# Kernel optimization log

Measured on AMD Instinct MI355X. Metric: run time of the kernel, lower is better.

Reference implementation:

```python
import jax, jax.numpy as jnp
import numpy as np
import math

NUM_BANDS = 16
BINS = 1024
CROPSIZE = 1024
BATCH = 4


def setup_inputs() -> dict:
    key = jax.random.key(0)
    ks = jax.random.split(key, 10)
    s = 1.0 / math.sqrt(BINS)
    return {
        "x": jax.random.normal(ks[0], (BATCH, CROPSIZE, BINS), jnp.float32),
        "Wq": jax.random.normal(ks[1], (BINS, BINS), jnp.float32) * s,
        "bq": jax.random.normal(ks[2], (BINS,), jnp.float32) * 0.02,
        "Wk": jax.random.normal(ks[3], (BINS, BINS), jnp.float32) * s,
        "bk": jax.random.normal(ks[4], (BINS,), jnp.float32) * 0.02,
        "Wv": jax.random.normal(ks[5], (BINS, BINS), jnp.float32) * s,
        "bv": jax.random.normal(ks[6], (BINS,), jnp.float32) * 0.02,
        "Wo": jax.random.normal(ks[7], (BINS, BINS), jnp.float32) * s,
        "bo": jax.random.normal(ks[8], (BINS,), jnp.float32) * 0.02,
        "er": jax.random.normal(ks[9], (BINS // NUM_BANDS, CROPSIZE), jnp.float32),
    }


def reference(x, Wq, bq, Wk, bk, Wv, bv, Wo, bo, er):
    b, w, c = x.shape
    h = NUM_BANDS
    d = c // h
    # Linear projections (torch Linear: x @ W.T + b)
    q = (jnp.einsum("bwc,oc->bwo", x, Wq) + bq).reshape(b, w, h, d).transpose(0, 2, 1, 3)  # [b,h,w,d]
    k = (jnp.einsum("bwc,oc->bwo", x, Wk) + bk).reshape(b, w, h, d).transpose(0, 2, 1, 3)  # [b,h,w,d]
    v = (jnp.einsum("bwc,oc->bwo", x, Wv) + bv).reshape(b, w, h, d).transpose(0, 2, 1, 3)  # [b,h,w,d]
    # relative-position bias via skew trick
    qe = jnp.einsum("bhwd,dc->bhwc", q, er)  # [b,h,w,cropsize]
    qe = jnp.pad(qe, ((0, 0), (0, 0), (0, 0), (1, 0)))  # pad last dim on left -> [b,h,w,crop+1]
    p = jnp.swapaxes(qe, 2, 3)[:, :, 1:, :]  # [b,h,crop,w] == [b,h,w,w] since crop==w
    qk = (jnp.einsum("bhwd,bhud->bhwu", q, k) + p) / math.sqrt(c)
    a = jax.nn.softmax(qk, axis=-1)
    av = jnp.einsum("bhwu,bhud->bhwd", a, v).transpose(0, 2, 1, 3).reshape(b, w, c)
    return jnp.einsum("bwc,oc->bwo", av, Wo) + bo
```

## Files before the change

kernel.cpp:

```cpp
#include <hip/hip_runtime.h>
#include <stdint.h>

typedef __attribute__((ext_vector_type(8))) short   short8;
typedef __attribute__((ext_vector_type(8))) __bf16  bf16x8;
typedef __attribute__((ext_vector_type(4))) float   floatx4;

__device__ __forceinline__ float bf2f(uint16_t h) {
    union { uint32_t u; float f; } v; v.u = ((uint32_t)h) << 16; return v.f;
}
__device__ __forceinline__ uint16_t f2bf(float f) {
    union { float f; uint32_t u; } v; v.f = f;
    uint32_t u = v.u;
    u += 0x7FFFu + ((u >> 16) & 1u);
    return (uint16_t)(u >> 16);
}
__device__ __forceinline__ floatx4 mfma16(short8 a, short8 b, floatx4 c) {
    return __builtin_amdgcn_mfma_f32_16x16x32_bf16(
        __builtin_bit_cast(bf16x8, a), __builtin_bit_cast(bf16x8, b), c, 0, 0, 0);
}
__device__ __forceinline__ void gll16(const short* g, short* l) {
    __builtin_amdgcn_global_load_lds(
        (const __attribute__((address_space(1))) uint32_t*)g,
        (__attribute__((address_space(3))) uint32_t*)l, 16, 0, 0);
}

__global__ void conv_all(
    const float* __restrict__ x,
    const float* __restrict__ Wq, const float* __restrict__ Wk,
    const float* __restrict__ Wv, const float* __restrict__ Wo,
    const float* __restrict__ bq, const float* __restrict__ bk,
    const float* __restrict__ bv, const float* __restrict__ bo,
    const float* __restrict__ er,
    short* __restrict__ xb, short* __restrict__ Wb,
    short* __restrict__ ball, short* __restrict__ ErT)
{
    int blk = blockIdx.x, tid = threadIdx.x;
    if (blk < 4096) {
        int i = blk * 256 + tid;
        float4 v = ((const float4*)x)[i];
        ((short4*)xb)[i] = make_short4((short)f2bf(v.x), (short)f2bf(v.y),
                                       (short)f2bf(v.z), (short)f2bf(v.w));
    } else if (blk < 8192) {
        int rel = blk - 4096;
        int wsel = rel >> 10;
        int i = (rel & 1023) * 256 + tid;
        const float* W = (wsel == 0) ? Wq : (wsel == 1) ? Wk : (wsel == 2) ? Wv : Wo;
        float4 v = ((const float4*)W)[i];
        ((short4*)(Wb + ((size_t)wsel << 20)))[i] =
            make_short4((short)f2bf(v.x), (short)f2bf(v.y),
                        (short)f2bf(v.z), (short)f2bf(v.w));
    } else if (blk < 8448) {
        int idx = (blk - 8192) * 256 + tid;
        int w = idx >> 6, d = idx & 63;
        ErT[idx] = (short)f2bf(er[d * 1024 + w]);
    } else {
        int idx = (blk - 8448) * 256 + tid;
        int sel = idx >> 10, j = idx & 1023;
        const float* s = (sel == 0) ? bq : (sel == 1) ? bk : (sel == 2) ? bv : bo;
        ball[idx] = (short)f2bf(s[j]);
    }
}

__device__ __forceinline__ void gemm_body(
    const short* __restrict__ A, const short* __restrict__ Wt,
    const short* __restrict__ bias, short* __restrict__ dst,
    float* __restrict__ dstf, int variant)
{
    __shared__ short As[128 * 64];
    __shared__ short Bs[128 * 64];
    const int tid  = threadIdx.x;
    const int wid  = tid >> 6;
    const int lane = tid & 63;
    const int m0 = blockIdx.x * 128;
    const int n0 = blockIdx.y * 128;
    const int wm = (wid >> 1) * 64;
    const int wn = (wid & 1) * 64;
    const int lrow = lane & 15;
    const int quad = lane >> 4;
    const int srow = lane >> 3;
    const int sscol = (((lane & 7) ^ (srow & 7)) << 3);
    const int rx = lrow & 7;

    floatx4 acc[4][4];
#pragma unroll
    for (int r = 0; r < 4; ++r)
#pragma unroll
        for (int c = 0; c < 4; ++c) acc[r][c] = (floatx4){0.f, 0.f, 0.f, 0.f};

    for (int k0 = 0; k0 < 1024; k0 += 64) {
#pragma unroll
        for (int i = 0; i < 4; ++i) {
            int q = wid * 4 + i;
            gll16(A + (size_t)(m0 + q * 8 + srow) * 1024 + k0 + sscol,
                  &As[q * 512 + lane * 8]);
        }
#pragma unroll
        for (int i = 0; i < 4; ++i) {
            int q = wid * 4 + i;
            gll16(Wt + (size_t)(n0 + q * 8 + srow) * 1024 + k0 + sscol,
                  &Bs[q * 512 + lane * 8]);
        }
        __syncthreads();
#pragma unroll
        for (int ks = 0; ks < 2; ++ks) {
            short8 af[4], bfr[4];
#pragma unroll
            for (int r = 0; r < 4; ++r)
                af[r] = *(const short8*)&As[(wm + r * 16 + lrow) * 64 +
                                            (((ks * 4 + quad) ^ rx) << 3)];
#pragma unroll
            for (int c = 0; c < 4; ++c)
                bfr[c] = *(const short8*)&Bs[(wn + c * 16 + lrow) * 64 +
                                             (((ks * 4 + quad) ^ rx) << 3)];
#pragma unroll
            for (int r = 0; r < 4; ++r)
#pragma unroll
                for (int c = 0; c < 4; ++c)
                    acc[r][c] = mfma16(af[r], bfr[c], acc[r][c]);
        }
        __syncthreads();
    }

#pragma unroll
    for (int c = 0; c < 4; ++c) {
        int col = n0 + wn + c * 16 + lrow;
        float bv = bf2f((uint16_t)bias[col]);
#pragma unroll
        for (int r = 0; r < 4; ++r) {
#pragma unroll
            for (int g = 0; g < 4; ++g) {
                int m = m0 + wm + r * 16 + quad * 4 + g;
                float fv = acc[r][c][g] + bv;
                if (variant == 3) {
                    dstf[(size_t)m * 1024 + col] = fv;
                } else if (variant == 2) {
                    int bh = (m >> 10) * 16 + (col >> 6);
                    dst[(size_t)bh * 65536 + (size_t)(col & 63) * 1024 + (m & 1023)] =
                        (short)f2bf(fv);
                } else {
                    int bh = (m >> 10) * 16 + (col >> 6);
                    dst[(size_t)bh * 65536 + (size_t)(m & 1023) * 64 + (col & 63)] =
                        (short)f2bf(fv);
                }
            }
        }
    }
}

__global__ __launch_bounds__(256) void out_gemm(
    const short* __restrict__ AV, const short* __restrict__ Wo,
    const short* __restrict__ bo, float* __restrict__ out)
{
    gemm_body(AV, Wo, bo, nullptr, out, 3);
}

#define VM0  asm volatile("s_waitcnt vmcnt(0)" ::: "memory")
#define BARR asm volatile("s_barrier" ::: "memory")

__device__ __forceinline__ void stage_unit(const short* src, short* region, int tid)
{
    const int row  = tid >> 3;
    const int scol = (((tid & 7) ^ (row & 7)) << 3);
    gll16(src + (size_t)row * 1024 + scol, region + tid * 8);
}

#define SAU(buf, u) (As + (buf) * 16384 + (u) * 4096)
#define SBU(buf, u) (Bs + (buf) * 12288 + (u) * 4096)
#define STG_A(buf, u, kt) stage_unit(Asrc + (size_t)(u) * 65536 + (size_t)(kt) * 64, SAU(buf, u), tid)
#define STG_B(buf, u, kt) stage_unit(Bsrc + (size_t)(u) * 65536 + (size_t)(kt) * 64, SBU(buf, u), tid)
#define STG7(buf, kt) do { \
    STG_A(buf, 0, kt); STG_A(buf, 1, kt); STG_A(buf, 2, kt); STG_A(buf, 3, kt); \
    STG_B(buf, 0, kt); STG_B(buf, 1, kt); STG_B(buf, 2, kt); } while (0)

#define RD_A(buf) do { \
    _Pragma("unroll") for (int fr_ = 0; fr_ < 8; ++fr_) { \
        const short* p_ = SAU(buf, wm * 2 + (fr_ >> 2)) + ((fr_ & 3) * 16 + lrow) * 64; \
        _Pragma("unroll") for (int ks_ = 0; ks_ < 2; ++ks_) \
            a[fr_][ks_] = *(const short8*)&p_[((ks_ * 4 + quad) ^ rx) << 3]; \
    } } while (0)

#define RD_B(buf, c) do { \
    const short* p_ = SBU(buf, c) + (wn * 16 + lrow) * 64; \
    _Pragma("unroll") for (int ks_ = 0; ks_ < 2; ++ks_) \
        bb[ks_] = *(const short8*)&p_[((ks_ * 4 + quad) ^ rx) << 3]; \
    } while (0)

#define MFMA_PH(c) do { \
    __builtin_amdgcn_s_setprio(1); \
    _Pragma("unroll") for (int ks_ = 0; ks_ < 2; ++ks_) \
        _Pragma("unroll") for (int fr_ = 0; fr_ < 8; ++fr_) \
            acc[fr_][c] = mfma16(a[fr_][ks_], bb[ks_], acc[fr_][c]); \
    __builtin_amdgcn_s_setprio(0); \
    } while (0)

__global__ __launch_bounds__(512, 2) void qkv_gemm2ph(
    const short* __restrict__ x, const short* __restrict__ Wb,
    const short* __restrict__ ball,
    short* __restrict__ Qb, short* __restrict__ Kb, short* __restrict__ Vb)
{
    extern __shared__ short lds[];
    short* As = lds;
    short* Bs = lds + 32768;
    const int tid  = threadIdx.x;
    const int wid  = tid >> 6;
    const int lane = tid & 63;
    const int wm   = wid >> 2;
    const int wn   = wid & 3;
    const int lrow = lane & 15;
    const int quad = lane >> 4;
    const int rx   = lrow & 7;
    const int bid  = blockIdx.x;
    const int swz  = (bid & 7) * 32 + (bid >> 3);
    const int mi   = swz & 15, ni = swz >> 4;
    const int m0   = mi * 256, n0 = ni * 192;
    const short* Asrc = x  + (size_t)m0 * 1024;
    const short* Bsrc = Wb + (size_t)n0 * 1024;

    floatx4 acc[8][3];
#pragma unroll
    for (int r = 0; r < 8; ++r)
#pragma unroll
        for (int c = 0; c < 3; ++c) acc[r][c] = (floatx4){0.f, 0.f, 0.f, 0.f};

    short8 a[8][2], bb[2];

    STG7(0, 0);
    VM0; BARR;

#pragma unroll 2
    for (int t = 0; t < 16; ++t) {
        const int cur = t & 1;
        if (t < 15) STG7(cur ^ 1, t + 1);
        RD_A(cur);
        RD_B(cur, 0); MFMA_PH(0);
        RD_B(cur, 1); MFMA_PH(1);
        RD_B(cur, 2); MFMA_PH(2);
        VM0; BARR;
    }

#pragma unroll
    for (int fc = 0; fc < 3; ++fc) {
        int col = n0 + fc * 64 + wn * 16 + lrow;
        int z   = col >> 10;
        int c1  = col & 1023;
        short* dst = (z == 0) ? Qb : (z == 1) ? Kb : Vb;
        float bv = bf2f((uint16_t)ball[col]);
#pragma unroll
        for (int fr = 0; fr < 8; ++fr) {
#pragma unroll
            for (int g = 0; g < 4; ++g) {
                int m = m0 + wm * 128 + fr * 16 + quad * 4 + g;
                float fv = acc[fr][fc][g] + bv;
                int bh = (m >> 10) * 16 + (c1 >> 6);
                if (z == 2)
                    dst[(size_t)bh * 65536 + (size_t)(c1 & 63) * 1024 + (m & 1023)] =
                        (short)f2bf(fv);
                else
                    dst[(size_t)bh * 65536 + (size_t)(m & 1023) * 64 + (c1 & 63)] =
                        (short)f2bf(fv);
            }
        }
    }
}

#define PSTR 72
__global__ __launch_bounds__(512, 4) void attn_kernel(
    const short* __restrict__ Q, const short* __restrict__ K,
    const short* __restrict__ Vt, const short* __restrict__ ErT,
    short* __restrict__ AV)
{
    __shared__ short smem[33792];
    short* Ks  = smem;
    short* Qks = smem + 8192;
    short* Vs  = smem + 16384;
    short* Ps  = smem + 24576;
    float* oaccS = (float*)smem;
    float* lrunS = ((float*)smem) + 128 * 65;

    const int tid  = threadIdx.x;
    const int wid  = tid >> 6;
    const int lane = tid & 63;
    const int rg   = wid >> 1;
    const int cg   = wid & 1;
    const int lrow = lane & 15;
    const int quad = lane >> 4;
    const int lk   = quad * 8;
    const int srow = lane >> 3;
    const int sscol = (((lane & 7) ^ (srow & 7)) << 3);
    const int rx = lrow & 7;
    const int h = blockIdx.x, b = blockIdx.y;
    const int bh = b * 16 + h;
    const int i0 = blockIdx.z * 128;
    const short* Qbh = Q  + (size_t)bh * 65536;
    const short* Kbh = K  + (size_t)bh * 65536;
    const short* Vbh = Vt + (size_t)bh * 65536;

    short8 qa[2][4];
#pragma unroll
    for (int m = 0; m < 2; ++m) {
        int row = i0 + rg * 32 + m * 16 + lrow;
#pragma unroll
        for (int kk = 0; kk < 2; ++kk) {
            qa[m][kk]     = *(const short8*)&Qbh[(size_t)row * 64 + kk * 32 + lk];
            qa[m][kk + 2] = *(const short8*)&ErT[(size_t)row * 64 + kk * 32 + lk];
        }
    }

    float lrun[2][4];
    floatx4 oacc[2][4];
#pragma unroll
    for (int m = 0; m < 2; ++m) {
#pragma unroll
        for (int g = 0; g < 4; ++g) lrun[m][g] = 0.f;
#pragma unroll
        for (int c = 0; c < 4; ++c) oacc[m][c] = (floatx4){0.f, 0.f, 0.f, 0.f};
    }

    gll16(Kbh + (size_t)(wid * 8 + srow) * 64 + sscol,    Ks  + wid * 512 + lane * 8);
    gll16(Qbh + (size_t)(wid * 8 + srow) * 64 + sscol,    Qks + wid * 512 + lane * 8);
    gll16(Vbh + (size_t)(wid * 8 + srow) * 1024 + sscol,  Vs  + wid * 512 + lane * 8);

    const float sc2 = 1.44269504088896f / 32.0f;

    for (int jt = 0; jt < 16; ++jt) {
        const int cur = jt & 1;
        __syncthreads();

        if (jt < 15) {
            int j1 = (jt + 1) * 64;
            gll16(Kbh + (size_t)(j1 + wid * 8 + srow) * 64 + sscol,    Ks  + (cur ^ 1) * 4096 + wid * 512 + lane * 8);
            gll16(Qbh + (size_t)(j1 + wid * 8 + srow) * 64 + sscol,    Qks + (cur ^ 1) * 4096 + wid * 512 + lane * 8);
            gll16(Vbh + (size_t)(wid * 8 + srow) * 1024 + j1 + sscol,  Vs  + (cur ^ 1) * 4096 + wid * 512 + lane * 8);
        }

        floatx4 s[2][2];
#pragma unroll
        for (int m = 0; m < 2; ++m)
#pragma unroll
            for (int c = 0; c < 2; ++c) s[m][c] = (floatx4){0.f, 0.f, 0.f, 0.f};
#pragma unroll
        for (int kk = 0; kk < 4; ++kk) {
            short8 kb[2];
            const short* src = ((kk < 2) ? Ks : Qks) + cur * 4096;
            const int kl = kk & 1;
#pragma unroll
            for (int c = 0; c < 2; ++c)
                kb[c] = *(const short8*)&src[(cg * 32 + c * 16 + lrow) * 64 +
                                             (((kl * 4 + quad) ^ rx) << 3)];
#pragma unroll
            for (int m = 0; m < 2; ++m)
#pragma unroll
                for (int c = 0; c < 2; ++c)
                    s[m][c] = mfma16(qa[m][kk], kb[c], s[m][c]);
        }

#pragma unroll
        for (int m = 0; m < 2; ++m)
#pragma unroll
            for (int c = 0; c < 2; ++c)
#pragma unroll
                for (int g = 0; g < 4; ++g)
                    s[m][c][g] = exp2f(s[m][c][g] * sc2);
#pragma unroll
        for (int m = 0; m < 2; ++m)
#pragma unroll
            for (int g = 0; g < 4; ++g)
                lrun[m][g] += s[m][0][g] + s[m][1][g];

#pragma unroll
        for (int m = 0; m < 2; ++m)
#pragma unroll
            for (int c = 0; c < 2; ++c)
#pragma unroll
                for (int g = 0; g < 4; ++g)
                    Ps[(rg * 32 + m * 16 + quad * 4 + g) * PSTR + cg * 32 + c * 16 + lrow] =
                        (short)f2bf(s[m][c][g]);
        __asm__ __volatile__("" ::: "memory");

        {
            short8 pa[2], vb[4];
#pragma unroll
            for (int m = 0; m < 2; ++m)
                pa[m] = *(const short8*)&Ps[(rg * 32 + m * 16 + lrow) * PSTR + cg * 32 + lk];
#pragma unroll
            for (int c = 0; c < 4; ++c)
                vb[c] = *(const short8*)&Vs[cur * 4096 + (c * 16 + lrow) * 64 +
                                            (((cg * 4 + quad) ^ rx) << 3)];
#pragma unroll
            for (int m = 0; m < 2; ++m)
#pragma unroll
                for (int c = 0; c < 4; ++c)
                    oacc[m][c] = mfma16(pa[m], vb[c], oacc[m][c]);
        }
    }

#pragma unroll
    for (int m = 0; m < 2; ++m)
#pragma unroll
        for (int g = 0; g < 4; ++g) {
            float r = lrun[m][g];
#pragma unroll
            for (int d = 1; d < 16; d <<= 1) r += __shfl_xor(r, d, 64);
            lrun[m][g] = r;
        }

    __syncthreads();
    if (cg == 0) {
#pragma unroll
        for (int m = 0; m < 2; ++m) {
#pragma unroll
            for (int c = 0; c < 4; ++c)
#pragma unroll
                for (int g = 0; g < 4; ++g)
                    oaccS[(rg * 32 + m * 16 + quad * 4 + g) * 65 + c * 16 + lrow] =
                        oacc[m][c][g];
            if (lrow == 0)
#pragma unroll
                for (int g = 0; g < 4; ++g)
                    lrunS[rg * 32 + m * 16 + quad * 4 + g] = lrun[m][g];
        }
    }
    __syncthreads();
    if (cg == 1) {
#pragma unroll
        for (int m = 0; m < 2; ++m)
#pragma unroll
            for (int g = 0; g < 4; ++g) {
                int row = rg * 32 + m * 16 + quad * 4 + g;
                float lt = lrun[m][g] + lrunS[row];
#pragma unroll
                for (int c = 0; c < 4; ++c) {
                    float tot = oacc[m][c][g] + oaccS[row * 65 + c * 16 + lrow];
                    AV[((size_t)b * 1024 + i0 + row) * 1024 + h * 64 + c * 16 + lrow] =
                        (short)f2bf(tot / lt);
                }
            }
    }
}

extern "C" void kernel_launch(void* const* d_in, const int* in_sizes, int n_in,
                              void* d_out, int out_size, void* d_ws, size_t ws_size,
                              hipStream_t stream) {
    const float* x  = (const float*)d_in[0];
    const float* Wq = (const float*)d_in[1];
    const float* bq = (const float*)d_in[2];
    const float* Wk = (const float*)d_in[3];
    const float* bk = (const float*)d_in[4];
    const float* Wv = (const float*)d_in[5];
    const float* bv = (const float*)d_in[6];
    const float* Wo = (const float*)d_in[7];
    const float* bo = (const float*)d_in[8];
    const float* er = (const float*)d_in[9];
    float* out = (float*)d_out;

    const size_t M1 = 1u << 20;
    short* ws   = (short*)d_ws;
    short* xb   = (short*)d_out;
    short* Qb   = ws;
    short* Kb   = ws + 4 * M1;
    short* Vb   = ws + 8 * M1;
    short* AVb  = ws + 12 * M1;
    short* Wb   = ws + 16 * M1;
    short* ball = ws + 20 * M1;
    short* ErT  = ws + 20 * M1 + 4096;

    static bool attr_done = false;
    if (!attr_done) {
        hipFuncSetAttribute((const void*)qkv_gemm2ph,
                            hipFuncAttributeMaxDynamicSharedMemorySize, 114688);
        attr_done = true;
    }

    hipLaunchKernelGGL(conv_all, dim3(8464), dim3(256), 0, stream,
                       x, Wq, Wk, Wv, Wo, bq, bk, bv, bo, er, xb, Wb, ball, ErT);
    hipLaunchKernelGGL(qkv_gemm2ph, dim3(256), dim3(512), 114688, stream,
                       xb, Wb, ball, Qb, Kb, Vb);
    hipLaunchKernelGGL(attn_kernel, dim3(16, 4, 8), dim3(512), 0, stream,
                       Qb, Kb, Vb, ErT, AVb);
    hipLaunchKernelGGL(out_gemm, dim3(32, 8), dim3(256), 0, stream,
                       AVb, Wb + 3 * M1, ball + 3072, out);
}
```

Before: 203.7 us.

## Replace output GEMM with double-buffered 512-thread kernel and XCD-aware tile mapping

Replaces the simple single-buffered 256-thread output projection GEMM with a 512-thread kernel. The new kernel prefetches the next K tile into a second LDS buffer while the current one is consumed by MFMAs, and raises wave priority around the MFMA bursts. It also remaps block IDs so blocks landing on the same XCD share A/B tiles in L2, and changes the QKV GEMM's tile mapping the same way. The aim is to hide global-load latency and improve L2 locality. The cost is more LDS per block and each wave holding a smaller 64x32 tile, which lowers MFMA reuse per LDS read.

```diff
diff --git a/kernel.cpp b/kernel.cpp
--- a/kernel.cpp
+++ b/kernel.cpp
@@ -61,99 +61,6 @@
     }
 }
 
-__device__ __forceinline__ void gemm_body(
-    const short* __restrict__ A, const short* __restrict__ Wt,
-    const short* __restrict__ bias, short* __restrict__ dst,
-    float* __restrict__ dstf, int variant)
-{
-    __shared__ short As[128 * 64];
-    __shared__ short Bs[128 * 64];
-    const int tid  = threadIdx.x;
-    const int wid  = tid >> 6;
-    const int lane = tid & 63;
-    const int m0 = blockIdx.x * 128;
-    const int n0 = blockIdx.y * 128;
-    const int wm = (wid >> 1) * 64;
-    const int wn = (wid & 1) * 64;
-    const int lrow = lane & 15;
-    const int quad = lane >> 4;
-    const int srow = lane >> 3;
-    const int sscol = (((lane & 7) ^ (srow & 7)) << 3);
-    const int rx = lrow & 7;
-
-    floatx4 acc[4][4];
-#pragma unroll
-    for (int r = 0; r < 4; ++r)
-#pragma unroll
-        for (int c = 0; c < 4; ++c) acc[r][c] = (floatx4){0.f, 0.f, 0.f, 0.f};
-
-    for (int k0 = 0; k0 < 1024; k0 += 64) {
-#pragma unroll
-        for (int i = 0; i < 4; ++i) {
-            int q = wid * 4 + i;
-            gll16(A + (size_t)(m0 + q * 8 + srow) * 1024 + k0 + sscol,
-                  &As[q * 512 + lane * 8]);
-        }
-#pragma unroll
-        for (int i = 0; i < 4; ++i) {
-            int q = wid * 4 + i;
-            gll16(Wt + (size_t)(n0 + q * 8 + srow) * 1024 + k0 + sscol,
-                  &Bs[q * 512 + lane * 8]);
-        }
-        __syncthreads();
-#pragma unroll
-        for (int ks = 0; ks < 2; ++ks) {
-            short8 af[4], bfr[4];
-#pragma unroll
-            for (int r = 0; r < 4; ++r)
-                af[r] = *(const short8*)&As[(wm + r * 16 + lrow) * 64 +
-                                            (((ks * 4 + quad) ^ rx) << 3)];
-#pragma unroll
-            for (int c = 0; c < 4; ++c)
-                bfr[c] = *(const short8*)&Bs[(wn + c * 16 + lrow) * 64 +
-                                             (((ks * 4 + quad) ^ rx) << 3)];
-#pragma unroll
-            for (int r = 0; r < 4; ++r)
-#pragma unroll
-                for (int c = 0; c < 4; ++c)
-                    acc[r][c] = mfma16(af[r], bfr[c], acc[r][c]);
-        }
-        __syncthreads();
-    }
-
-#pragma unroll
-    for (int c = 0; c < 4; ++c) {
-        int col = n0 + wn + c * 16 + lrow;
-        float bv = bf2f((uint16_t)bias[col]);
-#pragma unroll
-        for (int r = 0; r < 4; ++r) {
-#pragma unroll
-            for (int g = 0; g < 4; ++g) {
-                int m = m0 + wm + r * 16 + quad * 4 + g;
-                float fv = acc[r][c][g] + bv;
-                if (variant == 3) {
-                    dstf[(size_t)m * 1024 + col] = fv;
-                } else if (variant == 2) {
-                    int bh = (m >> 10) * 16 + (col >> 6);
-                    dst[(size_t)bh * 65536 + (size_t)(col & 63) * 1024 + (m & 1023)] =
-                        (short)f2bf(fv);
-                } else {
-                    int bh = (m >> 10) * 16 + (col >> 6);
-                    dst[(size_t)bh * 65536 + (size_t)(m & 1023) * 64 + (col & 63)] =
-                        (short)f2bf(fv);
-                }
-            }
-        }
-    }
-}
-
-__global__ __launch_bounds__(256) void out_gemm(
-    const short* __restrict__ AV, const short* __restrict__ Wo,
-    const short* __restrict__ bo, float* __restrict__ out)
-{
-    gemm_body(AV, Wo, bo, nullptr, out, 3);
-}
-
 #define VM0  asm volatile("s_waitcnt vmcnt(0)" ::: "memory")
 #define BARR asm volatile("s_barrier" ::: "memory")
 
@@ -210,8 +117,9 @@
     const int quad = lane >> 4;
     const int rx   = lrow & 7;
     const int bid  = blockIdx.x;
-    const int swz  = (bid & 7) * 32 + (bid >> 3);
-    const int mi   = swz & 15, ni = swz >> 4;
+    const int xcd  = bid & 7, gg = bid >> 3;
+    const int mi   = (xcd >> 1) * 4 + (gg & 3);
+    const int ni   = (xcd & 1) * 8 + (gg >> 2);
     const int m0   = mi * 256, n0 = ni * 192;
     const short* Asrc = x  + (size_t)m0 * 1024;
     const short* Bsrc = Wb + (size_t)n0 * 1024;
@@ -258,6 +166,93 @@
                 else
                     dst[(size_t)bh * 65536 + (size_t)(m & 1023) * 64 + (c1 & 63)] =
                         (short)f2bf(fv);
+            }
+        }
+    }
+}
+
+#define SAU2(buf, u) (As2 + (buf) * 8192 + (u) * 4096)
+#define SBU2(buf, u) (Bs2 + (buf) * 8192 + (u) * 4096)
+#define STG4(buf, kt) do { \
+    stage_unit(Asrc + 0 * 65536 + (size_t)(kt) * 64, SAU2(buf, 0), tid); \
+    stage_unit(Asrc + 1 * 65536 + (size_t)(kt) * 64, SAU2(buf, 1), tid); \
+    stage_unit(Bsrc + 0 * 65536 + (size_t)(kt) * 64, SBU2(buf, 0), tid); \
+    stage_unit(Bsrc + 1 * 65536 + (size_t)(kt) * 64, SBU2(buf, 1), tid); } while (0)
+
+#define RD_A2(buf) do { \
+    _Pragma("unroll") for (int fr_ = 0; fr_ < 4; ++fr_) { \
+        const short* p_ = SAU2(buf, wm) + (fr_ * 16 + lrow) * 64; \
+        _Pragma("unroll") for (int ks_ = 0; ks_ < 2; ++ks_) \
+            a[fr_][ks_] = *(const short8*)&p_[((ks_ * 4 + quad) ^ rx) << 3]; \
+    } } while (0)
+
+#define RD_B2(buf, c) do { \
+    const short* p_ = SBU2(buf, c) + (wn * 16 + lrow) * 64; \
+    _Pragma("unroll") for (int ks_ = 0; ks_ < 2; ++ks_) \
+        bb[ks_] = *(const short8*)&p_[((ks_ * 4 + quad) ^ rx) << 3]; \
+    } while (0)
+
+#define MFMA_PH2(c) do { \
+    __builtin_amdgcn_s_setprio(1); \
+    _Pragma("unroll") for (int ks_ = 0; ks_ < 2; ++ks_) \
+        _Pragma("unroll") for (int fr_ = 0; fr_ < 4; ++fr_) \
+            acc[fr_][c] = mfma16(a[fr_][ks_], bb[ks_], acc[fr_][c]); \
+    __builtin_amdgcn_s_setprio(0); \
+    } while (0)
+
+__global__ __launch_bounds__(512, 2) void out_gemm2ph(
+    const short* __restrict__ AV, const short* __restrict__ Wo,
+    const short* __restrict__ bo, float* __restrict__ out)
+{
+    __shared__ short As2[2 * 2 * 4096];
+    __shared__ short Bs2[2 * 2 * 4096];
+    const int tid  = threadIdx.x;
+    const int wid  = tid >> 6;
+    const int lane = tid & 63;
+    const int wm   = wid >> 2;
+    const int wn   = wid & 3;
+    const int lrow = lane & 15;
+    const int quad = lane >> 4;
+    const int rx   = lrow & 7;
+    const int bid  = blockIdx.x + blockIdx.y * 32;
+    const int xcd  = bid & 7, gg = bid >> 3;
+    const int mi   = (xcd & 3) * 8 + (gg & 7);
+    const int ni   = (xcd >> 2) * 4 + (gg >> 3);
+    const int m0   = mi * 128, n0 = ni * 128;
+    const short* Asrc = AV + (size_t)m0 * 1024;
+    const short* Bsrc = Wo + (size_t)n0 * 1024;
+
+    floatx4 acc[4][2];
+#pragma unroll
+    for (int r = 0; r < 4; ++r)
+#pragma unroll
+        for (int c = 0; c < 2; ++c) acc[r][c] = (floatx4){0.f, 0.f, 0.f, 0.f};
+
+    short8 a[4][2], bb[2];
+
+    STG4(0, 0);
+    VM0; BARR;
+
+#pragma unroll 2
+    for (int t = 0; t < 16; ++t) {
+        const int cur = t & 1;
+        if (t < 15) STG4(cur ^ 1, t + 1);
+        RD_A2(cur);
+        RD_B2(cur, 0); MFMA_PH2(0);
+        RD_B2(cur, 1); MFMA_PH2(1);
+        VM0; BARR;
+    }
+
+#pragma unroll
+    for (int fc = 0; fc < 2; ++fc) {
+        int col = n0 + fc * 64 + wn * 16 + lrow;
+        float bv = bf2f((uint16_t)bo[col]);
+#pragma unroll
+        for (int fr = 0; fr < 4; ++fr) {
+#pragma unroll
+            for (int g = 0; g < 4; ++g) {
+                int m = m0 + wm * 64 + fr * 16 + quad * 4 + g;
+                out[(size_t)m * 1024 + col] = acc[fr][fc][g] + bv;
             }
         }
     }
@@ -477,6 +472,6 @@
                        xb, Wb, ball, Qb, Kb, Vb);
     hipLaunchKernelGGL(attn_kernel, dim3(16, 4, 8), dim3(512), 0, stream,
                        Qb, Kb, Vb, ErT, AVb);
-    hipLaunchKernelGGL(out_gemm, dim3(32, 8), dim3(256), 0, stream,
+    hipLaunchKernelGGL(out_gemm2ph, dim3(32, 8), dim3(512), 0, stream,
                        AVb, Wb + 3 * M1, ball + 3072, out);
 }
```

Result: faster. 196.9 us (-3.3%).
